# Kernel tuning notes

Measured on AMD Instinct MI355X. Metric: run time of the kernel, lower is better.

## Reference

```python
import jax, jax.numpy as jnp
import numpy as np

H = 128  # hidden/input size fixed by module


def setup_inputs() -> dict:
    key = jax.random.key(0)
    ks = jax.random.split(key, 8)
    S, B = 512, 256
    scale = 1.0 / np.sqrt(H)
    return {
        "X": jax.random.normal(ks[0], (S, B, H), dtype=jnp.float32),
        "h": jax.random.normal(ks[1], (1, B, H), dtype=jnp.float32),
        "lin_W": jax.random.uniform(ks[2], (H, H), jnp.float32, -scale, scale),
        "lin_b": jax.random.uniform(ks[3], (H,), jnp.float32, -scale, scale),
        "W_ih": jax.random.uniform(ks[4], (3 * H, H), jnp.float32, -scale, scale),
        "W_hh": jax.random.uniform(ks[5], (3 * H, H), jnp.float32, -scale, scale),
        "b_ih": jax.random.uniform(ks[6], (3 * H,), jnp.float32, -scale, scale),
        "b_hh": jax.random.uniform(ks[7], (3 * H,), jnp.float32, -scale, scale),
    }


def reference(X, h, lin_W, lin_b, W_ih, W_hh, b_ih, b_hh):
    # Linear: y = X @ W^T + b   (torch nn.Linear convention)
    Xp = jnp.einsum("sbd,ed->sbe", X, lin_W) + lin_b
    # Precompute input-hidden gate projections for all timesteps: (S, B, 3H)
    gx_all = jnp.einsum("sbd,gd->sbg", Xp, W_ih) + b_ih

    def step(h_t, gx):
        gh = h_t @ W_hh.T + b_hh  # (B, 3H)
        xr, xz, xn = jnp.split(gx, 3, axis=-1)
        hr, hz, hn = jnp.split(gh, 3, axis=-1)
        r = jax.nn.sigmoid(xr + hr)
        z = jax.nn.sigmoid(xz + hz)
        n = jnp.tanh(xn + r * hn)
        h_new = (1.0 - z) * n + z * h_t
        return h_new, h_new

    _, outs = jax.lax.scan(step, h[0], gx_all)
    return outs  # (S, B, H) — the module returns only the output sequence
```

## Files before the change

### kernel.cpp

```cpp
#include <hip/hip_runtime.h>
#include <math.h>

#define HID 128
#define G3  384
#define BATCH 256
#define SEQ 512
#define NB 16
#define NBLK (BATCH/NB)

typedef __bf16 bf16x8 __attribute__((ext_vector_type(8)));
typedef __bf16 bf16x4 __attribute__((ext_vector_type(4)));
typedef float  f32x4  __attribute__((ext_vector_type(4)));

#define LOG2E 1.44269504088896f

__device__ __forceinline__ float sigm(float x) {
    return __builtin_amdgcn_rcpf(1.f + __builtin_amdgcn_exp2f(-LOG2E * x));
}
__device__ __forceinline__ float tanh_fast(float x) {
    float e = __builtin_amdgcn_exp2f(-2.f * LOG2E * x);
    return __builtin_amdgcn_rcpf(1.f + e) * 2.f - 1.f;
}
__device__ __forceinline__ f32x4 mfma16(bf16x8 a, bf16x8 b, f32x4 c) {
    return __builtin_amdgcn_mfma_f32_16x16x32_bf16(a, b, c, 0, 0, 0);
}
__device__ __forceinline__ bf16x8 cvt8(float4 a, float4 b) {
    bf16x8 f;
    f[0] = (__bf16)a.x; f[1] = (__bf16)a.y; f[2] = (__bf16)a.z; f[3] = (__bf16)a.w;
    f[4] = (__bf16)b.x; f[5] = (__bf16)b.y; f[6] = (__bf16)b.z; f[7] = (__bf16)b.w;
    return f;
}
__device__ __forceinline__ bf16x4 cvt4(float4 a) {
    bf16x4 f;
    f[0] = (__bf16)a.x; f[1] = (__bf16)a.y; f[2] = (__bf16)a.z; f[3] = (__bf16)a.w;
    return f;
}

__global__ void fold_kernel(const float* __restrict__ lin_W,
                            const float* __restrict__ lin_b,
                            const float* __restrict__ W_ih,
                            const float* __restrict__ b_ih,
                            float* __restrict__ Wc,
                            float* __restrict__ bcA) {
    const int g = blockIdx.x;
    const int d = threadIdx.x;
    float acc = 0.f;
    for (int e = 0; e < HID; ++e) acc += W_ih[g * HID + e] * lin_W[e * HID + d];
    Wc[g * HID + d] = acc;
    if (d == 0) {
        float b = 0.f;
        for (int e = 0; e < HID; ++e) b += W_ih[g * HID + e] * lin_b[e];
        bcA[g] = b + b_ih[g];
    }
}

__global__ __launch_bounds__(512, 2)
void gru_scan_mfma(const float* __restrict__ X,
                   const float* __restrict__ h0,
                   const float* __restrict__ W_hh,
                   const float* __restrict__ b_hh,
                   const float* __restrict__ Wc,
                   const float* __restrict__ bcA,
                   float* __restrict__ out) {
    const int t   = threadIdx.x;
    const int w   = t >> 6;
    const int l   = t & 63;
    const int col = l & 15;
    const int lr  = l >> 4;
    const int bb  = blockIdx.x * NB;

    __shared__ __align__(16) unsigned char lds[12288];
    unsigned char* hbuf  = lds;
    unsigned char* xbuf0 = lds + 4096;
    unsigned char* xbuf1 = lds + 8192;

    auto SW = [](int b, int off) { return b * 256 + (off ^ ((b & 7) << 4)); };

    bf16x8 aW[3][4], aC[3][4];
    #pragma unroll
    for (int g3 = 0; g3 < 3; ++g3)
        #pragma unroll
        for (int kt = 0; kt < 4; ++kt) {
            const int row = g3 * HID + w * 16 + col;
            const float* pw = W_hh + row * HID + kt * 32 + lr * 8;
            const float* pc = Wc   + row * HID + kt * 32 + lr * 8;
            aW[g3][kt] = cvt8(*(const float4*)pw, *(const float4*)(pw + 4));
            aC[g3][kt] = cvt8(*(const float4*)pc, *(const float4*)(pc + 4));
        }
    #pragma unroll
    for (int g3 = 0; g3 < 3; ++g3)
        #pragma unroll
        for (int kt = 0; kt < 4; ++kt) {
            asm volatile("" : "+v"(aW[g3][kt]));
            asm volatile("" : "+v"(aC[g3][kt]));
        }

    float br[4], bz[4], bnx[4], bnh[4];
    #pragma unroll
    for (int q = 0; q < 4; ++q) {
        const int g = w * 16 + lr * 4 + q;
        br[q]  = bcA[g] + b_hh[g];
        bz[q]  = bcA[HID + g] + b_hh[HID + g];
        bnx[q] = bcA[2 * HID + g];
        bnh[q] = b_hh[2 * HID + g];
    }

    f32x4 hold = *(const f32x4*)(h0 + (size_t)(bb + col) * HID + w * 16 + lr * 4);

    const int sb = t >> 5;
    const int sk = (t & 31) * 4;

    float4 xp, xq;
    if (t < 256) {
        const int hb = t >> 4, hk = (t & 15) * 8;
        const float* ph = h0 + (size_t)(bb + hb) * HID + hk;
        *(bf16x8*)(hbuf + SW(hb, hk * 2)) =
            cvt8(*(const float4*)ph, *(const float4*)(ph + 4));
    }
    {
        const float* px = X + ((size_t)0 * BATCH + bb + sb) * HID + sk;
        *(bf16x4*)(xbuf0 + SW(sb, sk * 2)) = cvt4(*(const float4*)px);
        const float* p1 = X + ((size_t)1 * BATCH + bb + sb) * HID + sk;
        xp = *(const float4*)p1;
    }
    __syncthreads();

    const f32x4 vzero = {0.f, 0.f, 0.f, 0.f};

    auto STEP = [&](int s, unsigned char* xcur, unsigned char* xnxt,
                    float4& xc, float4& xn) {
        bf16x8 Bh[4], Bx[4];
        #pragma unroll
        for (int kt = 0; kt < 4; ++kt) {
            Bh[kt] = *(const bf16x8*)(hbuf + SW(col, kt * 64 + lr * 16));
            Bx[kt] = *(const bf16x8*)(xcur + SW(col, kt * 64 + lr * 16));
        }
        {
            int sp = s + 2; if (sp > SEQ - 1) sp = SEQ - 1;
            const float* px = X + ((size_t)sp * BATCH + bb + sb) * HID + sk;
            xn = *(const float4*)px;
        }
        f32x4 ar = vzero, az = vzero, anh = vzero, anx = vzero;
        #pragma unroll
        for (int kt = 0; kt < 4; ++kt) {
            ar  = mfma16(aW[0][kt], Bh[kt], ar);
            ar  = mfma16(aC[0][kt], Bx[kt], ar);
            az  = mfma16(aW[1][kt], Bh[kt], az);
            az  = mfma16(aC[1][kt], Bx[kt], az);
            anh = mfma16(aW[2][kt], Bh[kt], anh);
            anx = mfma16(aC[2][kt], Bx[kt], anx);
        }
        __syncthreads();

        *(bf16x4*)(xnxt + SW(sb, sk * 2)) = cvt4(xc);

        f32x4 hnew;
        #pragma unroll
        for (int q = 0; q < 4; ++q) {
            float r = sigm(ar[q] + br[q]);
            float z = sigm(az[q] + bz[q]);
            float n = tanh_fast(anx[q] + bnx[q] + r * (anh[q] + bnh[q]));
            hnew[q] = n + z * (hold[q] - n);
        }
        hold = hnew;
        *(bf16x4*)(hbuf + SW(col, (w * 16 + lr * 4) * 2)) = cvt4(*(float4*)&hnew);
        float4 o; o.x = hnew[0]; o.y = hnew[1]; o.z = hnew[2]; o.w = hnew[3];
        *(float4*)(out + ((size_t)s * BATCH + bb + col) * HID + w * 16 + lr * 4) = o;

        __syncthreads();
    };

    for (int s0 = 0; s0 < SEQ; s0 += 2) {
        STEP(s0,     xbuf0, xbuf1, xp, xq);
        STEP(s0 + 1, xbuf1, xbuf0, xq, xp);
    }
}

extern "C" void kernel_launch(void* const* d_in, const int* in_sizes, int n_in,
                              void* d_out, int out_size, void* d_ws, size_t ws_size,
                              hipStream_t stream) {
    const float* X     = (const float*)d_in[0];
    const float* h0    = (const float*)d_in[1];
    const float* lin_W = (const float*)d_in[2];
    const float* lin_b = (const float*)d_in[3];
    const float* W_ih  = (const float*)d_in[4];
    const float* W_hh  = (const float*)d_in[5];
    const float* b_ih  = (const float*)d_in[6];
    const float* b_hh  = (const float*)d_in[7];
    float* out = (float*)d_out;

    float* Wc  = (float*)d_ws;
    float* bcA = Wc + G3 * HID;

    fold_kernel<<<G3, HID, 0, stream>>>(lin_W, lin_b, W_ih, b_ih, Wc, bcA);
    gru_scan_mfma<<<NBLK, 512, 0, stream>>>(X, h0, W_hh, b_hh, Wc, bcA, out);
}
```

Baseline: 439.1 us.

## Double-buffer hidden state in LDS to drop one barrier per GRU step

Adds a second LDS buffer for the hidden state so each step reads from one buffer and writes to the other. This removes the mid-step __syncthreads that separated the MFMA reads from the h/x writes, and moves the x staging write to the start of the step. The remaining barrier becomes an explicit lgkmcnt wait plus s_barrier, which no longer waits on outstanding global stores. Biases are folded into the MFMA accumulator initial values, trading a few adds for more LDS use and a reliance on hand-placed wait counts for correctness.

```diff
diff --git a/kernel.cpp b/kernel.cpp
--- a/kernel.cpp
+++ b/kernel.cpp
@@ -69,10 +69,11 @@
     const int lr  = l >> 4;
     const int bb  = blockIdx.x * NB;
 
-    __shared__ __align__(16) unsigned char lds[12288];
-    unsigned char* hbuf  = lds;
-    unsigned char* xbuf0 = lds + 4096;
-    unsigned char* xbuf1 = lds + 8192;
+    __shared__ __align__(16) unsigned char lds[16384];
+    unsigned char* hA = lds;
+    unsigned char* hB = lds + 4096;
+    unsigned char* xA = lds + 8192;
+    unsigned char* xB = lds + 12288;
 
     auto SW = [](int b, int off) { return b * 256 + (off ^ ((b & 7) << 4)); };
 
@@ -95,14 +96,14 @@
             asm volatile("" : "+v"(aC[g3][kt]));
         }
 
-    float br[4], bz[4], bnx[4], bnh[4];
+    f32x4 vbr, vbz, vbnx, vbnh;
     #pragma unroll
     for (int q = 0; q < 4; ++q) {
         const int g = w * 16 + lr * 4 + q;
-        br[q]  = bcA[g] + b_hh[g];
-        bz[q]  = bcA[HID + g] + b_hh[HID + g];
-        bnx[q] = bcA[2 * HID + g];
-        bnh[q] = b_hh[2 * HID + g];
+        vbr[q]  = bcA[g] + b_hh[g];
+        vbz[q]  = bcA[HID + g] + b_hh[HID + g];
+        vbnx[q] = bcA[2 * HID + g];
+        vbnh[q] = b_hh[2 * HID + g];
     }
 
     f32x4 hold = *(const f32x4*)(h0 + (size_t)(bb + col) * HID + w * 16 + lr * 4);
@@ -114,33 +115,37 @@
     if (t < 256) {
         const int hb = t >> 4, hk = (t & 15) * 8;
         const float* ph = h0 + (size_t)(bb + hb) * HID + hk;
-        *(bf16x8*)(hbuf + SW(hb, hk * 2)) =
+        *(bf16x8*)(hA + SW(hb, hk * 2)) =
             cvt8(*(const float4*)ph, *(const float4*)(ph + 4));
     }
     {
         const float* px = X + ((size_t)0 * BATCH + bb + sb) * HID + sk;
-        *(bf16x4*)(xbuf0 + SW(sb, sk * 2)) = cvt4(*(const float4*)px);
+        *(bf16x4*)(xA + SW(sb, sk * 2)) = cvt4(*(const float4*)px);
         const float* p1 = X + ((size_t)1 * BATCH + bb + sb) * HID + sk;
         xp = *(const float4*)p1;
     }
-    __syncthreads();
-
-    const f32x4 vzero = {0.f, 0.f, 0.f, 0.f};
-
-    auto STEP = [&](int s, unsigned char* xcur, unsigned char* xnxt,
+    asm volatile("s_waitcnt lgkmcnt(0)" ::: "memory");
+    __builtin_amdgcn_s_barrier();
+
+    auto STEP = [&](int s, unsigned char* hR, unsigned char* hW,
+                    unsigned char* xR, unsigned char* xW,
                     float4& xc, float4& xn) {
-        bf16x8 Bh[4], Bx[4];
-        #pragma unroll
-        for (int kt = 0; kt < 4; ++kt) {
-            Bh[kt] = *(const bf16x8*)(hbuf + SW(col, kt * 64 + lr * 16));
-            Bx[kt] = *(const bf16x8*)(xcur + SW(col, kt * 64 + lr * 16));
-        }
+        *(bf16x4*)(xW + SW(sb, sk * 2)) = cvt4(xc);
+
         {
             int sp = s + 2; if (sp > SEQ - 1) sp = SEQ - 1;
             const float* px = X + ((size_t)sp * BATCH + bb + sb) * HID + sk;
             xn = *(const float4*)px;
         }
-        f32x4 ar = vzero, az = vzero, anh = vzero, anx = vzero;
+
+        bf16x8 Bh[4], Bx[4];
+        #pragma unroll
+        for (int kt = 0; kt < 4; ++kt) {
+            Bh[kt] = *(const bf16x8*)(hR + SW(col, kt * 64 + lr * 16));
+            Bx[kt] = *(const bf16x8*)(xR + SW(col, kt * 64 + lr * 16));
+        }
+
+        f32x4 ar = vbr, az = vbz, anh = vbnh, anx = vbnx;
         #pragma unroll
         for (int kt = 0; kt < 4; ++kt) {
             ar  = mfma16(aW[0][kt], Bh[kt], ar);
@@ -150,29 +155,27 @@
             anh = mfma16(aW[2][kt], Bh[kt], anh);
             anx = mfma16(aC[2][kt], Bx[kt], anx);
         }
-        __syncthreads();
-
-        *(bf16x4*)(xnxt + SW(sb, sk * 2)) = cvt4(xc);
 
         f32x4 hnew;
         #pragma unroll
         for (int q = 0; q < 4; ++q) {
-            float r = sigm(ar[q] + br[q]);
-            float z = sigm(az[q] + bz[q]);
-            float n = tanh_fast(anx[q] + bnx[q] + r * (anh[q] + bnh[q]));
+            float r = sigm(ar[q]);
+            float z = sigm(az[q]);
+            float n = tanh_fast(anx[q] + r * anh[q]);
             hnew[q] = n + z * (hold[q] - n);
         }
         hold = hnew;
-        *(bf16x4*)(hbuf + SW(col, (w * 16 + lr * 4) * 2)) = cvt4(*(float4*)&hnew);
+        *(bf16x4*)(hW + SW(col, (w * 16 + lr * 4) * 2)) = cvt4(*(float4*)&hnew);
         float4 o; o.x = hnew[0]; o.y = hnew[1]; o.z = hnew[2]; o.w = hnew[3];
         *(float4*)(out + ((size_t)s * BATCH + bb + col) * HID + w * 16 + lr * 4) = o;
 
-        __syncthreads();
+        asm volatile("s_waitcnt lgkmcnt(0)" ::: "memory");
+        __builtin_amdgcn_s_barrier();
     };
 
     for (int s0 = 0; s0 < SEQ; s0 += 2) {
-        STEP(s0,     xbuf0, xbuf1, xp, xq);
-        STEP(s0 + 1, xbuf1, xbuf0, xq, xp);
+        STEP(s0,     hA, hB, xA, xB, xp, xq);
+        STEP(s0 + 1, hB, hA, xB, xA, xq, xp);
     }
 }
 
```

After: 439.1 us. About the same (+0.0%).
